# Performance work log

Measured on AMD Instinct MI355X. Metric: run time of the kernel, lower is better.

Reference implementation:

```python
import jax, jax.numpy as jnp
import numpy as np

# ---- static config (matches init_kwargs) ----
B, L, D, H, NC = 2, 4096, 256, 8, 3
TOP_N, R = 8, 32              # top_n, vicinity_radius
LS, LE = 1000, 3000           # label_start, label_end
NL = 2                        # n_cross_attn_layers
FF = 4 * D                    # ffn_expand * d_model
Q_MAX = 2 * TOP_N * (2 * R + 1)  # 1040
HD = D // H


def setup_inputs() -> dict:
    key = jax.random.key(0)
    ks = jax.random.split(key, 12)
    def rn(k, shape, s=0.05):
        return jax.random.normal(k, shape, jnp.float32) * s
    return {
        "encoder_output": jax.random.normal(ks[0], (B, L, D), jnp.float32),
        "coarse_logits": jax.random.normal(ks[1], (B, L, NC), jnp.float32),
        "ln_q_g": jnp.ones((NL, D), jnp.float32),
        "ln_q_b": jnp.zeros((NL, D), jnp.float32),
        "ln_kv_g": jnp.ones((NL, D), jnp.float32),
        "ln_kv_b": jnp.zeros((NL, D), jnp.float32),
        "Wq": rn(ks[2], (NL, D, D)), "bq": jnp.zeros((NL, D), jnp.float32),
        "Wk": rn(ks[3], (NL, D, D)), "bk": jnp.zeros((NL, D), jnp.float32),
        "Wv": rn(ks[4], (NL, D, D)), "bv": jnp.zeros((NL, D), jnp.float32),
        "Wo": rn(ks[5], (NL, D, D)), "bo": jnp.zeros((NL, D), jnp.float32),
        "ffn_g": jnp.ones((NL, D), jnp.float32),
        "ffn_b": jnp.zeros((NL, D), jnp.float32),
        "W1": rn(ks[6], (NL, D, FF)), "b1": jnp.zeros((NL, FF), jnp.float32),
        "W2": rn(ks[7], (NL, FF, D)), "b2": jnp.zeros((NL, D), jnp.float32),
        "head_W": rn(ks[8], (D, NC)), "head_b": jnp.zeros((NC,), jnp.float32),
    }


def _layer_norm(x, g, b, eps=1e-5):
    m = jnp.mean(x, axis=-1, keepdims=True)
    v = jnp.mean(jnp.square(x - m), axis=-1, keepdims=True)
    return (x - m) * jax.lax.rsqrt(v + eps) * g + b


def _select_vicinities(coarse_logits):
    # eval mode: no gumbel noise. Returns (vicinity_idx (B,Q_MAX) int32 with
    # sentinel L at pad/dup slots, q_pad_mask (B,Q_MAX) bool).
    lp = jax.nn.log_softmax(coarse_logits.astype(jnp.float32), axis=-1)
    pos = jnp.arange(L)
    region = (pos >= LS) & (pos < LE)
    acc = jnp.where(region, lp[..., 1], -jnp.inf)
    don = jnp.where(region, lp[..., 2], -jnp.inf)
    _, don_idx = jax.lax.top_k(don, TOP_N)
    _, acc_idx = jax.lax.top_k(acc, TOP_N)
    centers = jnp.concatenate([don_idx, acc_idx], axis=-1)        # (B, 2*TOP_N)
    offsets = jnp.arange(-R, R + 1)
    vic = jnp.clip(centers[:, :, None] + offsets, 0, L - 1).reshape(B, -1)
    s = jnp.sort(vic, axis=-1)
    is_first = jnp.concatenate(
        [jnp.ones((B, 1), bool), s[:, 1:] != s[:, :-1]], axis=-1)
    idx = jnp.where(is_first, s, L)  # sentinel L -> zero row of scratch
    return idx, is_first


def reference(encoder_output, coarse_logits, ln_q_g, ln_q_b, ln_kv_g, ln_kv_b,
              Wq, bq, Wk, bk, Wv, bv, Wo, bo, ffn_g, ffn_b, W1, b1, W2, b2,
              head_W, head_b):
    idx, mask = _select_vicinities(coarse_logits)      # torch.no_grad() region
    idx = jax.lax.stop_gradient(idx)
    mask = jax.lax.stop_gradient(mask)

    scratch = jnp.pad(encoder_output, ((0, 0), (0, 1), (0, 0)))   # (B, L+1, D)
    q_stream = jnp.take_along_axis(scratch, idx[:, :, None], axis=1)  # (B,Q,D)
    kv = encoder_output
    m3 = mask[:, :, None]

    for i in range(NL):
        q_in = _layer_norm(q_stream, ln_q_g[i], ln_q_b[i])
        kv_in = _layer_norm(kv, ln_kv_g[i], ln_kv_b[i])
        q = (q_in @ Wq[i] + bq[i]).reshape(B, Q_MAX, H, HD)
        k = (kv_in @ Wk[i] + bk[i]).reshape(B, L, H, HD)
        v = (kv_in @ Wv[i] + bv[i]).reshape(B, L, H, HD)
        scores = jnp.einsum('bqhd,bkhd->bhqk', q, k) / jnp.sqrt(
            jnp.float32(HD))
        attn = jax.nn.softmax(scores, axis=-1)
        ao = jnp.einsum('bhqk,bkhd->bqhd', attn, v).reshape(B, Q_MAX, D)
        q_stream = q_stream + ao @ Wo[i] + bo[i]
        q_stream = jnp.where(m3, q_stream, 0.0)
        h = _layer_norm(q_stream, ffn_g[i], ffn_b[i])
        h = jax.nn.gelu(h @ W1[i] + b1[i], approximate=False) @ W2[i] + b2[i]
        q_stream = jnp.where(m3, q_stream + h, 0.0)

    out_scratch = scratch.at[jnp.arange(B)[:, None], idx].set(q_stream)
    refined = out_scratch[:, :L]                                  # drop sentinel
    refined_logits = refined @ head_W + head_b                    # (B, L, 3)
    return refined_logits
```

## Files before the change

### kernel.cpp

```cpp
#include <hip/hip_runtime.h>
#include <cmath>

constexpr int B = 2, L = 4096, D = 256, H = 8, NC = 3;
constexpr int TOP_N = 8, R = 32;
constexpr int LS = 1000, LE = 3000;
constexpr int NL = 2;
constexpr int FF = 4 * D;
constexpr int Q_MAX = 2 * TOP_N * (2 * R + 1);
constexpr int HD = D / H;
constexpr int QROWS = B * Q_MAX;
constexpr int KVROWS = B * L;
constexpr int NQT = (Q_MAX + 31) / 32;
constexpr int NREG = LE - LS;
constexpr int NSPLIT = 8;
constexpr int KCHUNK = L / NSPLIT;
constexpr int NT = KCHUNK / 32;

typedef __attribute__((ext_vector_type(8))) short bf16x8;
typedef __attribute__((ext_vector_type(4))) float f32x4;
typedef __attribute__((ext_vector_type(4))) int i32x4;
typedef unsigned short u16;

union fr {
  bf16x8 h;
  i32x4 i;
};

__device__ __forceinline__ u16 f2bs(float f) {
  unsigned int u = __float_as_uint(f);
  unsigned int r = u + 0x7fffu + ((u >> 16) & 1u);
  return (u16)(r >> 16);
}
__device__ __forceinline__ float bs2f(u16 s) {
  return __uint_as_float(((unsigned int)s) << 16);
}
__device__ __forceinline__ float gelu_exact(float x) {
  return 0.5f * x * (1.f + erff(x * 0.70710678118654752440f));
}
__device__ __forceinline__ unsigned cvt_pk(float lo, float hi) {
  unsigned r;
  asm("v_cvt_pk_bf16_f32 %0, %1, %2" : "=v"(r) : "v"(lo), "v"(hi));
  return r;
}

#define GLL16(gsrc, ldst)                                                   \
  __builtin_amdgcn_global_load_lds(                                         \
      (const __attribute__((address_space(1))) unsigned int*)(gsrc),        \
      (__attribute__((address_space(3))) unsigned int*)(ldst), 16, 0, 0)

__global__ __launch_bounds__(1024) void select_kernel(
    const float* __restrict__ logits, int* __restrict__ idx_out,
    int* __restrict__ mask_out) {
  int b = blockIdx.x;
  int tid = threadIdx.x;
  __shared__ float vv[2][NREG];
  __shared__ int centers[2 * TOP_N];
  __shared__ unsigned present[L / 32];
  __shared__ float wred[16];
  __shared__ int wredi[16];
  __shared__ int offs[128];
  __shared__ int wtot[2];

  for (int p = tid; p < NREG; p += 1024) {
    const float* lg = logits + ((long)b * L + LS + p) * NC;
    float x0 = lg[0], x1 = lg[1], x2 = lg[2];
    float m = fmaxf(x0, fmaxf(x1, x2));
    float lse = m + logf(expf(x0 - m) + expf(x1 - m) + expf(x2 - m));
    vv[0][p] = x2 - lse;
    vv[1][p] = x1 - lse;
  }
  if (tid < 128) present[tid] = 0;
  __syncthreads();

  for (int sel = 0; sel < 2; ++sel) {
    for (int t = 0; t < TOP_N; ++t) {
      float bv = -INFINITY;
      int bi = 0x7fffffff;
      for (int p = tid; p < NREG; p += 1024) {
        float x = vv[sel][p];
        if (x > bv || (x == bv && p < bi)) { bv = x; bi = p; }
      }
#pragma unroll
      for (int off = 32; off; off >>= 1) {
        float ov = __shfl_xor(bv, off, 64);
        int oi = __shfl_xor(bi, off, 64);
        if (ov > bv || (ov == bv && oi < bi)) { bv = ov; bi = oi; }
      }
      if ((tid & 63) == 0) { wred[tid >> 6] = bv; wredi[tid >> 6] = bi; }
      __syncthreads();
      if (tid < 64) {
        bv = (tid < 16) ? wred[tid] : -INFINITY;
        bi = (tid < 16) ? wredi[tid] : 0x7fffffff;
#pragma unroll
        for (int off = 8; off; off >>= 1) {
          float ov = __shfl_xor(bv, off, 64);
          int oi = __shfl_xor(bi, off, 64);
          if (ov > bv || (ov == bv && oi < bi)) { bv = ov; bi = oi; }
        }
        if (tid == 0) {
          centers[sel * TOP_N + t] = LS + bi;
          vv[sel][bi] = -INFINITY;
        }
      }
      __syncthreads();
    }
  }

  for (int j = tid; j < Q_MAX; j += 1024) {
    int c = centers[j / (2 * R + 1)];
    int off = j % (2 * R + 1) - R;
    int v = c + off;
    v = v < 0 ? 0 : (v > L - 1 ? L - 1 : v);
    atomicOr(&present[v >> 5], 1u << (v & 31));
  }
  __syncthreads();

  int cnt = (tid < 128) ? __popc(present[tid]) : 0;
  if (tid < 128) {
    int x = cnt;
#pragma unroll
    for (int off = 1; off < 64; off <<= 1) {
      int o = __shfl_up(x, off, 64);
      if ((tid & 63) >= off) x += o;
    }
    if ((tid & 63) == 63) wtot[tid >> 6] = x;
    offs[tid] = x - cnt;
  }
  __syncthreads();
  int total = wtot[0] + wtot[1];
  if (tid < 128) {
    int base = offs[tid] + ((tid >= 64) ? wtot[0] : 0);
    unsigned mword = present[tid];
    while (mword) {
      int i = __ffs(mword) - 1;
      mword &= mword - 1;
      idx_out[b * Q_MAX + base] = tid * 32 + i;
      mask_out[b * Q_MAX + base] = 1;
      ++base;
    }
  }
  for (int j = total + tid; j < Q_MAX; j += 1024) {
    idx_out[b * Q_MAX + j] = L;
    mask_out[b * Q_MAX + j] = 0;
  }
}

__global__ __launch_bounds__(256) void gather_kernel(
    const float* __restrict__ enc, const int* __restrict__ idx,
    float* __restrict__ q_stream) {
  int row = blockIdx.x;
  int b = row / Q_MAX;
  int p = idx[row];
  float v = 0.f;
  if (p < L) v = enc[((long)b * L + p) * D + threadIdx.x];
  q_stream[(long)row * D + threadIdx.x] = v;
}

__global__ __launch_bounds__(256) void ln_bf16(
    const float* __restrict__ in, u16* __restrict__ out,
    const float* __restrict__ gg, const float* __restrict__ bb) {
  long row = blockIdx.x;
  int tid = threadIdx.x;
  float x = in[row * D + tid];
  float s1 = x, s2 = x * x;
#pragma unroll
  for (int off = 32; off; off >>= 1) {
    s1 += __shfl_xor(s1, off, 64);
    s2 += __shfl_xor(s2, off, 64);
  }
  __shared__ float p1[4], p2[4];
  int w = tid >> 6;
  if ((tid & 63) == 0) { p1[w] = s1; p2[w] = s2; }
  __syncthreads();
  s1 = p1[0] + p1[1] + p1[2] + p1[3];
  s2 = p2[0] + p2[1] + p2[2] + p2[3];
  float mean = s1 * (1.f / D);
  float var = fmaxf(s2 * (1.f / D) - mean * mean, 0.f);
  float r = rsqrtf(var + 1e-5f);
  out[row * D + tid] = f2bs((x - mean) * r * gg[tid] + bb[tid]);
}

__global__ __launch_bounds__(256) void ln_kv2(
    const float* __restrict__ in, u16* __restrict__ o0, u16* __restrict__ o1,
    const float* __restrict__ gg, const float* __restrict__ bb) {
  long row = blockIdx.x;
  int tid = threadIdx.x;
  float x = in[row * D + tid];
  float s1 = x, s2 = x * x;
#pragma unroll
  for (int off = 32; off; off >>= 1) {
    s1 += __shfl_xor(s1, off, 64);
    s2 += __shfl_xor(s2, off, 64);
  }
  __shared__ float p1[4], p2[4];
  int w = tid >> 6;
  if ((tid & 63) == 0) { p1[w] = s1; p2[w] = s2; }
  __syncthreads();
  s1 = p1[0] + p1[1] + p1[2] + p1[3];
  s2 = p2[0] + p2[1] + p2[2] + p2[3];
  float mean = s1 * (1.f / D);
  float var = fmaxf(s2 * (1.f / D) - mean * mean, 0.f);
  float r = rsqrtf(var + 1e-5f);
  float xn = (x - mean) * r;
  o0[row * D + tid] = f2bs(xn * gg[tid] + bb[tid]);
  o1[row * D + tid] = f2bs(xn * gg[D + tid] + bb[D + tid]);
}

__global__ __launch_bounds__(256) void transpose_tiled(
    const float* __restrict__ Wq_, const float* __restrict__ Wk_,
    const float* __restrict__ Wv_, const float* __restrict__ Wo_,
    const float* __restrict__ W1_, const float* __restrict__ W2_,
    u16* __restrict__ WT) {
  __shared__ u16 T[64][65];
  const long DD = (long)D * D, DFF = (long)D * FF;
  const long LSTR = 4 * DD + 2 * DFF;
  int t = blockIdx.x;
  int l = t / 192, r = t % 192;
  const float* src;
  long dbase;
  int K_, N_, kt, nt;
  if (r < 64) {
    int which = r >> 4, sub = r & 15;
    kt = sub >> 2;
    nt = sub & 3;
    K_ = 256;
    N_ = 256;
    src = (which == 0 ? Wk_ : which == 1 ? Wv_ : which == 2 ? Wq_ : Wo_) +
          (long)l * DD;
    dbase = (long)l * LSTR + (long)which * DD;
  } else if (r < 128) {
    int sub = r - 64;
    kt = sub >> 4;
    nt = sub & 15;
    K_ = 256;
    N_ = 1024;
    src = W1_ + (long)l * DFF;
    dbase = (long)l * LSTR + 4 * DD;
  } else {
    int sub = r - 128;
    kt = sub >> 2;
    nt = sub & 3;
    K_ = 1024;
    N_ = 256;
    src = W2_ + (long)l * DFF;
    dbase = (long)l * LSTR + 4 * DD + DFF;
  }
  int k0 = kt * 64, n0 = nt * 64;
  {
    int kr = threadIdx.x >> 2, c16 = (threadIdx.x & 3) * 16;
    const float* sp = src + (long)(k0 + kr) * N_ + n0 + c16;
#pragma unroll
    for (int i = 0; i < 4; ++i) {
      float4 v = *reinterpret_cast<const float4*>(sp + 4 * i);
      T[kr][c16 + 4 * i + 0] = f2bs(v.x);
      T[kr][c16 + 4 * i + 1] = f2bs(v.y);
      T[kr][c16 + 4 * i + 2] = f2bs(v.z);
      T[kr][c16 + 4 * i + 3] = f2bs(v.w);
    }
  }
  __syncthreads();
  {
    int nr = threadIdx.x >> 2, kc = (threadIdx.x & 3) * 16;
    u16 tmp[16];
#pragma unroll
    for (int j = 0; j < 16; ++j) tmp[j] = T[kc + j][nr];
    u16* dp = WT + dbase + (long)(n0 + nr) * K_ + k0 + kc;
    *reinterpret_cast<bf16x8*>(dp) = *reinterpret_cast<const bf16x8*>(&tmp[0]);
    *reinterpret_cast<bf16x8*>(dp + 8) =
        *reinterpret_cast<const bf16x8*>(&tmp[8]);
  }
}

template <int EPI>
__global__ __launch_bounds__(256) void gemm_mfma(
    const u16* __restrict__ A, const u16* __restrict__ BT,
    const float* __restrict__ bias, void* __restrict__ Cv,
    const float* __restrict__ resid, const int* __restrict__ mask, int M,
    int N, int K) {
  __shared__ short As[64][40];
  __shared__ short Bs[64][40];
  int bm = blockIdx.y * 64, bn = blockIdx.x * 64;
  int tid = threadIdx.x;
  int lane = tid & 63, w = tid >> 6;
  int g = lane >> 4, li = lane & 15;
  int wr = w >> 1, wc = w & 1;
  f32x4 acc[2][2] = {};

  int srow = tid >> 2, skc = (tid & 3) * 8;
  for (int k0 = 0; k0 < K; k0 += 32) {
    {
      int grow = bm + srow;
      bf16x8 av = {};
      if (grow < M)
        av = *reinterpret_cast<const bf16x8*>(A + (long)grow * K + k0 + skc);
      *reinterpret_cast<bf16x8*>(&As[srow][skc]) = av;
      bf16x8 bv = *reinterpret_cast<const bf16x8*>(
          BT + (long)(bn + srow) * K + k0 + skc);
      *reinterpret_cast<bf16x8*>(&Bs[srow][skc]) = bv;
    }
    __syncthreads();
    bf16x8 a0 = *reinterpret_cast<const bf16x8*>(&As[wr * 32 + li][g * 8]);
    bf16x8 a1 = *reinterpret_cast<const bf16x8*>(&As[wr * 32 + 16 + li][g * 8]);
    bf16x8 b0 = *reinterpret_cast<const bf16x8*>(&Bs[wc * 32 + li][g * 8]);
    bf16x8 b1 = *reinterpret_cast<const bf16x8*>(&Bs[wc * 32 + 16 + li][g * 8]);
    acc[0][0] = __builtin_amdgcn_mfma_f32_16x16x32_bf16(a0, b0, acc[0][0], 0, 0, 0);
    acc[0][1] = __builtin_amdgcn_mfma_f32_16x16x32_bf16(a0, b1, acc[0][1], 0, 0, 0);
    acc[1][0] = __builtin_amdgcn_mfma_f32_16x16x32_bf16(a1, b0, acc[1][0], 0, 0, 0);
    acc[1][1] = __builtin_amdgcn_mfma_f32_16x16x32_bf16(a1, b1, acc[1][1], 0, 0, 0);
    __syncthreads();
  }

#pragma unroll
  for (int mr = 0; mr < 2; ++mr)
#pragma unroll
    for (int nr = 0; nr < 2; ++nr)
#pragma unroll
      for (int r = 0; r < 4; ++r) {
        int row = bm + wr * 32 + mr * 16 + g * 4 + r;
        int col = bn + wc * 32 + nr * 16 + li;
        if (row >= M) continue;
        float v = acc[mr][nr][r] + bias[col];
        if (EPI == 1) v = gelu_exact(v);
        if (EPI == 2) {
          v += resid[(long)row * N + col];
          v = mask[row] ? v : 0.f;
          ((float*)Cv)[(long)row * N + col] = v;
        } else {
          ((u16*)Cv)[(long)row * N + col] = f2bs(v);
        }
      }
}

__global__ __launch_bounds__(256) void gemm_kv(
    const u16* __restrict__ A, const u16* __restrict__ BT,
    const float* __restrict__ biasK, const float* __restrict__ biasV,
    u16* __restrict__ Kh, u16* __restrict__ Vh) {
  __shared__ short As[64][40];
  __shared__ short Bs[64][40];
  int bm = blockIdx.y * 64, bn = blockIdx.x * 64;
  int tid = threadIdx.x;
  int lane = tid & 63, w = tid >> 6;
  int g = lane >> 4, li = lane & 15;
  int wr = w >> 1, wc = w & 1;
  f32x4 acc[2][2] = {};

  int srow = tid >> 2, skc = (tid & 3) * 8;
  for (int k0 = 0; k0 < D; k0 += 32) {
    {
      bf16x8 av = *reinterpret_cast<const bf16x8*>(
          A + (long)(bm + srow) * D + k0 + skc);
      *reinterpret_cast<bf16x8*>(&As[srow][skc]) = av;
      bf16x8 bv = *reinterpret_cast<const bf16x8*>(
          BT + (long)(bn + srow) * D + k0 + skc);
      *reinterpret_cast<bf16x8*>(&Bs[srow][skc]) = bv;
    }
    __syncthreads();
    bf16x8 a0 = *reinterpret_cast<const bf16x8*>(&As[wr * 32 + li][g * 8]);
    bf16x8 a1 = *reinterpret_cast<const bf16x8*>(&As[wr * 32 + 16 + li][g * 8]);
    bf16x8 b0 = *reinterpret_cast<const bf16x8*>(&Bs[wc * 32 + li][g * 8]);
    bf16x8 b1 = *reinterpret_cast<const bf16x8*>(&Bs[wc * 32 + 16 + li][g * 8]);
    acc[0][0] = __builtin_amdgcn_mfma_f32_16x16x32_bf16(a0, b0, acc[0][0], 0, 0, 0);
    acc[0][1] = __builtin_amdgcn_mfma_f32_16x16x32_bf16(a0, b1, acc[0][1], 0, 0, 0);
    acc[1][0] = __builtin_amdgcn_mfma_f32_16x16x32_bf16(a1, b0, acc[1][0], 0, 0, 0);
    acc[1][1] = __builtin_amdgcn_mfma_f32_16x16x32_bf16(a1, b1, acc[1][1], 0, 0, 0);
    __syncthreads();
  }

  if (bn < 256) {
    __shared__ u16 Ct[64][72];
#pragma unroll
    for (int mr = 0; mr < 2; ++mr)
#pragma unroll
      for (int nr = 0; nr < 2; ++nr)
#pragma unroll
        for (int r = 0; r < 4; ++r) {
          int rowL = wr * 32 + mr * 16 + g * 4 + r;
          int colL = wc * 32 + nr * 16 + li;
          Ct[rowL][colL] = f2bs(acc[mr][nr][r] + biasK[bn + colL]);
        }
    __syncthreads();
#pragma unroll
    for (int p = 0; p < 2; ++p) {
      int rowL = (tid >> 3) + p * 32;
      int c8 = (tid & 7) * 8;
      int grow = bm + rowL;
      int b2 = grow >> 12, key = grow & (L - 1);
      int gcol = bn + c8;
      int hh = gcol >> 5, dd = gcol & (HD - 1);
      int cst = (dd >> 3) ^ ((key >> 1) & 3);
      u16* dst = Kh + (((long)(b2 * H + hh) * L + key) * 32 + (cst << 3));
      *reinterpret_cast<bf16x8*>(dst) =
          *reinterpret_cast<const bf16x8*>(&Ct[rowL][c8]);
    }
  } else {
    int vbn = bn - 256;
    __shared__ u16 Ct[64][72];
#pragma unroll
    for (int mr = 0; mr < 2; ++mr)
#pragma unroll
      for (int nr = 0; nr < 2; ++nr)
#pragma unroll
        for (int r = 0; r < 4; ++r) {
          int rowL = wr * 32 + mr * 16 + g * 4 + r;
          int colL = wc * 32 + nr * 16 + li;
          Ct[colL][rowL] = f2bs(acc[mr][nr][r] + biasV[vbn + colL]);
        }
    __syncthreads();
    int b2 = bm >> 12;
#pragma unroll
    for (int p = 0; p < 2; ++p) {
      int colL = (tid >> 3) + p * 32;
      int rem = tid & 7;
      int kb = rem >> 2, k8 = (rem & 3) * 8;
      int gcol = vbn + colL;
      int hh = gcol >> 5, dd = gcol & (HD - 1);
      int kb32 = ((bm & (L - 1)) >> 5) + kb;
      int j = (k8 >> 2) ^ ((dd >> 1) & 6);
      u16* dst = Vh + (((long)(b2 * H + hh) * (L / 32) + kb32) * 1024 +
                       dd * 32 + (j << 2));
      *reinterpret_cast<bf16x8*>(dst) =
          *reinterpret_cast<const bf16x8*>(&Ct[colL][kb * 32 + k8]);
    }
  }
}

constexpr int POOLSZ = NSPLIT * 32 * 33 * 4 + NSPLIT * 32 * 4;

__global__ __launch_bounds__(512) void attn_mfma(
    const u16* __restrict__ Qb, const u16* __restrict__ Kh,
    const u16* __restrict__ Vh, u16* __restrict__ AO) {
  __shared__ alignas(16) char pool[POOLSZ];
  int i = blockIdx.x;
  int xcd = i & 7, slot = i >> 3;
  int bh = (xcd << 1) | (slot >= NQT ? 1 : 0);
  int qt = (slot >= NQT) ? slot - NQT : slot;
  int h = bh & 7;
  int b = bh >> 3;
  int tid = threadIdx.x, w = tid >> 6, lane = tid & 63;
  int g = lane >> 4, li = lane & 15;

  fr qf0, qf1;
  {
    const float QSC = 0.25509836048f;
#pragma unroll
    for (int qb = 0; qb < 2; ++qb) {
      int qrow = qt * 32 + qb * 16 + li;
      if (qrow >= Q_MAX) qrow = Q_MAX - 1;
      bf16x8 raw = *reinterpret_cast<const bf16x8*>(
          Qb + ((long)(b * Q_MAX + qrow)) * D + h * HD + g * 8);
      fr& qf = qb ? qf1 : qf0;
#pragma unroll
      for (int j = 0; j < 4; ++j)
        qf.i[j] = (int)cvt_pk(bs2f((u16)raw[2 * j]) * QSC,
                              bs2f((u16)raw[2 * j + 1]) * QSC);
    }
  }

  f32x4 acc00 = {}, acc01 = {}, acc10 = {}, acc11 = {};
  float den0 = 0.f, den1 = 0.f;
  const f32x4 z = {};

  const u16* kbase = Kh + ((long)(b * H + h) * L) * HD;
  const u16* vbase = Vh + ((long)(b * H + h) * L) * HD;
  int kstart = w * KCHUNK;
  char* wbase = pool + w * 4096;

  int s_li = (li >> 1) & 3;
  int t_li = (li >> 1) & 6;
  int kof0 = li * 32 + ((g ^ s_li) << 3);
  int kof1 = (16 + li) * 32 + ((g ^ s_li) << 3);
  int va0o = li * 32 + ((g ^ t_li) << 2);
  int vb0o = li * 32 + (((4 + g) ^ t_li) << 2);
  int va1o = (16 + li) * 32 + ((g ^ t_li) << 2);
  int vb1o = (16 + li) * 32 + (((4 + g) ^ t_li) << 2);

  for (int t = 0; t < NT; ++t) {
    {
      const u16* ks = kbase + (long)(kstart + t * 32) * HD + lane * 8;
      const u16* vs = vbase + (long)(kstart + t * 32) * HD + lane * 8;
      u16* lk = (u16*)wbase;
      asm volatile("s_waitcnt lgkmcnt(0)" ::: "memory");
      GLL16(ks, lk);
      GLL16(ks + 512, lk + 512);
      GLL16(vs, lk + 1024);
      GLL16(vs + 512, lk + 1536);
      asm volatile("s_waitcnt vmcnt(0)" ::: "memory");
      __builtin_amdgcn_sched_barrier(0);
    }

    const u16* kl = (const u16*)wbase;
    const u16* vl = kl + 1024;
    bf16x8 kf0 = *reinterpret_cast<const bf16x8*>(kl + kof0);
    bf16x8 kf1 = *reinterpret_cast<const bf16x8*>(kl + kof1);
    uint2 va0 = *reinterpret_cast<const uint2*>(vl + va0o);
    uint2 vb0 = *reinterpret_cast<const uint2*>(vl + vb0o);
    uint2 va1 = *reinterpret_cast<const uint2*>(vl + va1o);
    uint2 vb1 = *reinterpret_cast<const uint2*>(vl + vb1o);

    f32x4 s00 = __builtin_amdgcn_mfma_f32_16x16x32_bf16(kf0, qf0.h, z, 0, 0, 0);
    f32x4 s10 = __builtin_amdgcn_mfma_f32_16x16x32_bf16(kf1, qf0.h, z, 0, 0, 0);
    f32x4 s01 = __builtin_amdgcn_mfma_f32_16x16x32_bf16(kf0, qf1.h, z, 0, 0, 0);
    f32x4 s11 = __builtin_amdgcn_mfma_f32_16x16x32_bf16(kf1, qf1.h, z, 0, 0, 0);

    float p00[4], p10[4], p01[4], p11[4];
#pragma unroll
    for (int r = 0; r < 4; ++r) {
      p00[r] = exp2f(s00[r]);
      p10[r] = exp2f(s10[r]);
      p01[r] = exp2f(s01[r]);
      p11[r] = exp2f(s11[r]);
      den0 += p00[r] + p10[r];
      den1 += p01[r] + p11[r];
    }
    fr pf0, pf1;
    pf0.i[0] = (int)cvt_pk(p00[0], p00[1]);
    pf0.i[1] = (int)cvt_pk(p00[2], p00[3]);
    pf0.i[2] = (int)cvt_pk(p10[0], p10[1]);
    pf0.i[3] = (int)cvt_pk(p10[2], p10[3]);
    pf1.i[0] = (int)cvt_pk(p01[0], p01[1]);
    pf1.i[1] = (int)cvt_pk(p01[2], p01[3]);
    pf1.i[2] = (int)cvt_pk(p11[0], p11[1]);
    pf1.i[3] = (int)cvt_pk(p11[2], p11[3]);

    fr v0, v1;
    v0.i = (i32x4){(int)va0.x, (int)va0.y, (int)vb0.x, (int)vb0.y};
    v1.i = (i32x4){(int)va1.x, (int)va1.y, (int)vb1.x, (int)vb1.y};
    acc00 = __builtin_amdgcn_mfma_f32_16x16x32_bf16(v0.h, pf0.h, acc00, 0, 0, 0);
    acc01 = __builtin_amdgcn_mfma_f32_16x16x32_bf16(v0.h, pf1.h, acc01, 0, 0, 0);
    acc10 = __builtin_amdgcn_mfma_f32_16x16x32_bf16(v1.h, pf0.h, acc10, 0, 0, 0);
    acc11 = __builtin_amdgcn_mfma_f32_16x16x32_bf16(v1.h, pf1.h, acc11, 0, 0, 0);
  }

  den0 += __shfl_xor(den0, 16, 64);
  den0 += __shfl_xor(den0, 32, 64);
  den1 += __shfl_xor(den1, 16, 64);
  den1 += __shfl_xor(den1, 32, 64);

  __syncthreads();
  float (*accs)[32][33] = (float(*)[32][33])pool;
  float (*dsh)[32] = (float(*)[32])(pool + NSPLIT * 32 * 33 * 4);
#pragma unroll
  for (int r = 0; r < 4; ++r) {
    accs[w][g * 4 + r][li] = acc00[r];
    accs[w][g * 4 + r][16 + li] = acc01[r];
    accs[w][16 + g * 4 + r][li] = acc10[r];
    accs[w][16 + g * 4 + r][16 + li] = acc11[r];
  }
  if (g == 0) {
    dsh[w][li] = den0;
    dsh[w][16 + li] = den1;
  }
  __syncthreads();

  int q = tid >> 4, dp = tid & 15;
  float Den = 0.f, o0 = 0.f, o1 = 0.f;
#pragma unroll
  for (int ww = 0; ww < NSPLIT; ++ww) {
    Den += dsh[ww][q];
    o0 += accs[ww][2 * dp][q];
    o1 += accs[ww][2 * dp + 1][q];
  }
  float inv = 1.f / Den;
  int qrow = qt * 32 + q;
  if (qrow < Q_MAX) {
    unsigned pk = cvt_pk(o0 * inv, o1 * inv);
    *reinterpret_cast<unsigned*>(
        AO + ((long)(b * Q_MAX + qrow)) * D + h * HD + 2 * dp) = pk;
  }
}

__global__ __launch_bounds__(256) void head_kernel(
    const float* __restrict__ enc, const float* __restrict__ hW,
    const float* __restrict__ hb, float* __restrict__ out) {
  int row = blockIdx.x * 4 + (threadIdx.x >> 6);
  int lane = threadIdx.x & 63;
  const float4 a = *reinterpret_cast<const float4*>(enc + (long)row * D + lane * 4);
  float c0 = 0.f, c1 = 0.f, c2 = 0.f;
  const float av[4] = {a.x, a.y, a.z, a.w};
#pragma unroll
  for (int i = 0; i < 4; ++i) {
    int k = lane * 4 + i;
    c0 += av[i] * hW[k * 3];
    c1 += av[i] * hW[k * 3 + 1];
    c2 += av[i] * hW[k * 3 + 2];
  }
#pragma unroll
  for (int off = 32; off; off >>= 1) {
    c0 += __shfl_down(c0, off, 64);
    c1 += __shfl_down(c1, off, 64);
    c2 += __shfl_down(c2, off, 64);
  }
  if (lane == 0) {
    out[(long)row * 3] = c0 + hb[0];
    out[(long)row * 3 + 1] = c1 + hb[1];
    out[(long)row * 3 + 2] = c2 + hb[2];
  }
}

__global__ __launch_bounds__(64) void overwrite_kernel(
    const float* __restrict__ q_stream, const int* __restrict__ idx,
    const int* __restrict__ mask, const float* __restrict__ hW,
    const float* __restrict__ hb, float* __restrict__ out) {
  int j = blockIdx.x;
  if (!mask[j]) return;
  int b = j / Q_MAX;
  int p = idx[j];
  int lane = threadIdx.x;
  const float* a = q_stream + (long)j * D;
  float a0 = a[lane], a1 = a[lane + 64], a2 = a[lane + 128],
        a3 = a[lane + 192];
  for (int c = 0; c < 3; ++c) {
    float s = a0 * hW[lane * 3 + c] + a1 * hW[(lane + 64) * 3 + c] +
              a2 * hW[(lane + 128) * 3 + c] + a3 * hW[(lane + 192) * 3 + c];
    for (int off = 32; off > 0; off >>= 1) s += __shfl_down(s, off, 64);
    if (lane == 0) out[((long)b * L + p) * 3 + c] = s + hb[c];
  }
}

extern "C" void kernel_launch(void* const* d_in, const int* in_sizes, int n_in,
                              void* d_out, int out_size, void* d_ws,
                              size_t ws_size, hipStream_t stream) {
  const float* enc = (const float*)d_in[0];
  const float* clog = (const float*)d_in[1];
  const float* ln_q_g = (const float*)d_in[2];
  const float* ln_q_b = (const float*)d_in[3];
  const float* ln_kv_g = (const float*)d_in[4];
  const float* ln_kv_b = (const float*)d_in[5];
  const float* Wq = (const float*)d_in[6];
  const float* bq = (const float*)d_in[7];
  const float* Wk = (const float*)d_in[8];
  const float* bk = (const float*)d_in[9];
  const float* Wv = (const float*)d_in[10];
  const float* bv = (const float*)d_in[11];
  const float* Wo = (const float*)d_in[12];
  const float* bo = (const float*)d_in[13];
  const float* ffn_g = (const float*)d_in[14];
  const float* ffn_b = (const float*)d_in[15];
  const float* W1 = (const float*)d_in[16];
  const float* b1 = (const float*)d_in[17];
  const float* W2 = (const float*)d_in[18];
  const float* b2 = (const float*)d_in[19];
  const float* head_W = (const float*)d_in[20];
  const float* head_b = (const float*)d_in[21];
  float* out = (float*)d_out;

  char* ws = (char*)d_ws;
  float* q_stream = (float*)ws;            ws += (long)QROWS * D * 4;
  u16* kvl0 = (u16*)ws;                    ws += (long)KVROWS * D * 2;
  u16* kvl1 = (u16*)ws;                    ws += (long)KVROWS * D * 2;
  u16* Khbuf = (u16*)ws;                   ws += (long)B * H * L * HD * 2;
  u16* Vhbuf = (u16*)ws;                   ws += (long)B * H * L * HD * 2;
  u16* q_ln = (u16*)ws;                    ws += (long)QROWS * D * 2;
  u16* Qbuf = (u16*)ws;                    ws += (long)QROWS * D * 2;
  u16* AObuf = (u16*)ws;                   ws += (long)QROWS * D * 2;
  u16* H1buf = (u16*)ws;                   ws += (long)QROWS * FF * 2;
  u16* WT = (u16*)ws;                      ws += (long)NL * (4 * D * D + 2 * D * FF) * 2;
  int* idxbuf = (int*)ws;                  ws += QROWS * 4;
  int* maskbuf = (int*)ws;

  const long DD = (long)D * D, DFF = (long)D * FF;
  const long LSTR = 4 * DD + 2 * DFF;

  transpose_tiled<<<NL * 192, 256, 0, stream>>>(Wq, Wk, Wv, Wo, W1, W2, WT);
  ln_kv2<<<KVROWS, 256, 0, stream>>>(enc, kvl0, kvl1, ln_kv_g, ln_kv_b);
  select_kernel<<<B, 1024, 0, stream>>>(clog, idxbuf, maskbuf);
  gather_kernel<<<QROWS, 256, 0, stream>>>(enc, idxbuf, q_stream);

  for (int l = 0; l < NL; ++l) {
    u16* base = WT + l * LSTR;
    u16* kv_ln = (l == 0) ? kvl0 : kvl1;

    ln_bf16<<<QROWS, 256, 0, stream>>>(q_stream, q_ln, ln_q_g + l * D, ln_q_b + l * D);

    dim3 gKV(512 / 64, KVROWS / 64);
    gemm_kv<<<gKV, 256, 0, stream>>>(kv_ln, base, bk + l * D, bv + l * D,
                                     Khbuf, Vhbuf);
    dim3 gQ(D / 64, (QROWS + 63) / 64);
    gemm_mfma<0><<<gQ, 256, 0, stream>>>(q_ln, base + 2 * DD, bq + l * D,
                                         (void*)Qbuf, nullptr, nullptr,
                                         QROWS, D, D);

    attn_mfma<<<B * H * NQT, 512, 0, stream>>>(Qbuf, Khbuf, Vhbuf, AObuf);

    gemm_mfma<2><<<gQ, 256, 0, stream>>>(AObuf, base + 3 * DD, bo + l * D,
                                         (void*)q_stream, q_stream, maskbuf,
                                         QROWS, D, D);

    ln_bf16<<<QROWS, 256, 0, stream>>>(q_stream, q_ln, ffn_g + l * D, ffn_b + l * D);
    dim3 gF1(FF / 64, (QROWS + 63) / 64);
    gemm_mfma<1><<<gF1, 256, 0, stream>>>(q_ln, base + 4 * DD, b1 + l * FF,
                                          (void*)H1buf, nullptr, nullptr,
                                          QROWS, FF, D);
    dim3 gF2(D / 64, (QROWS + 63) / 64);
    gemm_mfma<2><<<gF2, 256, 0, stream>>>(H1buf, base + 4 * DD + DFF,
                                          b2 + l * D, (void*)q_stream,
                                          q_stream, maskbuf, QROWS, D, FF);
  }

  head_kernel<<<KVROWS / 4, 256, 0, stream>>>(enc, head_W, head_b, out);
  overwrite_kernel<<<QROWS, 64, 0, stream>>>(q_stream, idxbuf, maskbuf, head_W,
                                             head_b, out);
}
```

Before: 241.0 us.

## Merge Q projection into KV projection launch and speed up top-k selection

The K/V projection GEMM and the Q projection GEMM now run in one launch over a flat block grid, where each block picks its operands and epilogue from its block index. This removes one kernel launch per layer and lets the small Q GEMM run alongside the large K/V GEMM. The top-k selection is also rewritten: each wavefront keeps its values in registers and finds its local top-8 using shuffles, then one wavefront merges the 128 candidates. This replaces 16 block-wide barrier rounds over shared memory.

Measured after the change: 230.5 us. 1.05x faster.

```diff
diff --git a/kernel.cpp b/kernel.cpp
--- a/kernel.cpp
+++ b/kernel.cpp
@@ -15,6 +15,8 @@
 constexpr int NSPLIT = 8;
 constexpr int KCHUNK = L / NSPLIT;
 constexpr int NT = KCHUNK / 32;
+constexpr int KVBLK = 8 * (KVROWS / 64);
+constexpr int QBLK = 4 * ((QROWS + 63) / 64);
 
 typedef __attribute__((ext_vector_type(8))) short bf16x8;
 typedef __attribute__((ext_vector_type(4))) float f32x4;
@@ -53,57 +55,76 @@
     int* __restrict__ mask_out) {
   int b = blockIdx.x;
   int tid = threadIdx.x;
-  __shared__ float vv[2][NREG];
+  int w = tid >> 6, lane = tid & 63;
+  __shared__ float candv[16][8];
+  __shared__ int candi[16][8];
   __shared__ int centers[2 * TOP_N];
   __shared__ unsigned present[L / 32];
-  __shared__ float wred[16];
-  __shared__ int wredi[16];
   __shared__ int offs[128];
   __shared__ int wtot[2];
 
-  for (int p = tid; p < NREG; p += 1024) {
-    const float* lg = logits + ((long)b * L + LS + p) * NC;
-    float x0 = lg[0], x1 = lg[1], x2 = lg[2];
-    float m = fmaxf(x0, fmaxf(x1, x2));
-    float lse = m + logf(expf(x0 - m) + expf(x1 - m) + expf(x2 - m));
-    vv[0][p] = x2 - lse;
-    vv[1][p] = x1 - lse;
+  float vd[2], va[2];
+  int pidx[2];
+#pragma unroll
+  for (int j = 0; j < 2; ++j) {
+    int p = tid + j * 1024;
+    pidx[j] = p;
+    if (p < NREG) {
+      const float* lg = logits + ((long)b * L + LS + p) * NC;
+      float x0 = lg[0], x1 = lg[1], x2 = lg[2];
+      float m = fmaxf(x0, fmaxf(x1, x2));
+      float lse = m + logf(expf(x0 - m) + expf(x1 - m) + expf(x2 - m));
+      vd[j] = x2 - lse;
+      va[j] = x1 - lse;
+    } else {
+      vd[j] = -INFINITY;
+      va[j] = -INFINITY;
+    }
   }
   if (tid < 128) present[tid] = 0;
-  __syncthreads();
 
   for (int sel = 0; sel < 2; ++sel) {
-    for (int t = 0; t < TOP_N; ++t) {
-      float bv = -INFINITY;
-      int bi = 0x7fffffff;
-      for (int p = tid; p < NREG; p += 1024) {
-        float x = vv[sel][p];
-        if (x > bv || (x == bv && p < bi)) { bv = x; bi = p; }
+    float v0 = (sel == 0) ? vd[0] : va[0];
+    float v1 = (sel == 0) ? vd[1] : va[1];
+#pragma unroll
+    for (int r = 0; r < TOP_N; ++r) {
+      float mv;
+      int mi;
+      if (v0 >= v1) { mv = v0; mi = pidx[0]; }
+      else { mv = v1; mi = pidx[1]; }
+#pragma unroll
+      for (int off = 32; off; off >>= 1) {
+        float ov = __shfl_xor(mv, off, 64);
+        int oi = __shfl_xor(mi, off, 64);
+        if (ov > mv || (ov == mv && oi < mi)) { mv = ov; mi = oi; }
       }
-#pragma unroll
-      for (int off = 32; off; off >>= 1) {
-        float ov = __shfl_xor(bv, off, 64);
-        int oi = __shfl_xor(bi, off, 64);
-        if (ov > bv || (ov == bv && oi < bi)) { bv = ov; bi = oi; }
+      if (pidx[0] == mi) v0 = -INFINITY;
+      if (pidx[1] == mi) v1 = -INFINITY;
+      if (lane == 0) { candv[w][r] = mv; candi[w][r] = mi; }
+    }
+    __syncthreads();
+    if (tid < 64) {
+      int j0 = tid, j1 = tid + 64;
+      float c0 = candv[j0 >> 3][j0 & 7], c1 = candv[j1 >> 3][j1 & 7];
+      int i0 = candi[j0 >> 3][j0 & 7], i1 = candi[j1 >> 3][j1 & 7];
+#pragma unroll
+      for (int r = 0; r < TOP_N; ++r) {
+        float mv;
+        int mi;
+        if (c0 > c1 || (c0 == c1 && i0 < i1)) { mv = c0; mi = i0; }
+        else { mv = c1; mi = i1; }
+#pragma unroll
+        for (int off = 32; off; off >>= 1) {
+          float ov = __shfl_xor(mv, off, 64);
+          int oi = __shfl_xor(mi, off, 64);
+          if (ov > mv || (ov == mv && oi < mi)) { mv = ov; mi = oi; }
+        }
+        if (i0 == mi) c0 = -INFINITY;
+        if (i1 == mi) c1 = -INFINITY;
+        if (tid == 0) centers[sel * TOP_N + r] = LS + mi;
       }
-      if ((tid & 63) == 0) { wred[tid >> 6] = bv; wredi[tid >> 6] = bi; }
-      __syncthreads();
-      if (tid < 64) {
-        bv = (tid < 16) ? wred[tid] : -INFINITY;
-        bi = (tid < 16) ? wredi[tid] : 0x7fffffff;
-#pragma unroll
-        for (int off = 8; off; off >>= 1) {
-          float ov = __shfl_xor(bv, off, 64);
-          int oi = __shfl_xor(bi, off, 64);
-          if (ov > bv || (ov == bv && oi < bi)) { bv = ov; bi = oi; }
-        }
-        if (tid == 0) {
-          centers[sel * TOP_N + t] = LS + bi;
-          vv[sel][bi] = -INFINITY;
-        }
-      }
-      __syncthreads();
-    }
+    }
+    __syncthreads();
   }
 
   for (int j = tid; j < Q_MAX; j += 1024) {
@@ -331,24 +352,48 @@
       }
 }
 
-__global__ __launch_bounds__(256) void gemm_kv(
-    const u16* __restrict__ A, const u16* __restrict__ BT,
-    const float* __restrict__ biasK, const float* __restrict__ biasV,
-    u16* __restrict__ Kh, u16* __restrict__ Vh) {
+__global__ __launch_bounds__(256) void gemm_proj(
+    const u16* __restrict__ Akv, const u16* __restrict__ Aq,
+    const u16* __restrict__ WTbase, const float* __restrict__ biasK,
+    const float* __restrict__ biasV, const float* __restrict__ biasQ,
+    u16* __restrict__ Kh, u16* __restrict__ Vh, u16* __restrict__ Qb) {
   __shared__ short As[64][40];
   __shared__ short Bs[64][40];
-  int bm = blockIdx.y * 64, bn = blockIdx.x * 64;
+  __shared__ u16 Ct[64][72];
+  int bid = blockIdx.x;
   int tid = threadIdx.x;
   int lane = tid & 63, w = tid >> 6;
   int g = lane >> 4, li = lane & 15;
   int wr = w >> 1, wc = w & 1;
   f32x4 acc[2][2] = {};
+  const long DD = (long)D * D;
+
+  bool isKV = bid < KVBLK;
+  int bm, bn, M;
+  const u16* A;
+  const u16* BT;
+  if (isKV) {
+    bn = (bid & 7) * 64;
+    bm = (bid >> 3) * 64;
+    M = KVROWS;
+    A = Akv;
+    BT = WTbase;
+  } else {
+    int qb = bid - KVBLK;
+    bn = (qb & 3) * 64;
+    bm = (qb >> 2) * 64;
+    M = QROWS;
+    A = Aq;
+    BT = WTbase + 2 * DD;
+  }
 
   int srow = tid >> 2, skc = (tid & 3) * 8;
   for (int k0 = 0; k0 < D; k0 += 32) {
     {
-      bf16x8 av = *reinterpret_cast<const bf16x8*>(
-          A + (long)(bm + srow) * D + k0 + skc);
+      int grow = bm + srow;
+      bf16x8 av = {};
+      if (grow < M)
+        av = *reinterpret_cast<const bf16x8*>(A + (long)grow * D + k0 + skc);
       *reinterpret_cast<bf16x8*>(&As[srow][skc]) = av;
       bf16x8 bv = *reinterpret_cast<const bf16x8*>(
           BT + (long)(bn + srow) * D + k0 + skc);
@@ -366,8 +411,19 @@
     __syncthreads();
   }
 
-  if (bn < 256) {
-    __shared__ u16 Ct[64][72];
+  if (!isKV) {
+#pragma unroll
+    for (int mr = 0; mr < 2; ++mr)
+#pragma unroll
+      for (int nr = 0; nr < 2; ++nr)
+#pragma unroll
+        for (int r = 0; r < 4; ++r) {
+          int row = bm + wr * 32 + mr * 16 + g * 4 + r;
+          int col = bn + wc * 32 + nr * 16 + li;
+          if (row >= M) continue;
+          Qb[(long)row * D + col] = f2bs(acc[mr][nr][r] + biasQ[col]);
+        }
+  } else if (bn < 256) {
 #pragma unroll
     for (int mr = 0; mr < 2; ++mr)
 #pragma unroll
@@ -394,7 +450,6 @@
     }
   } else {
     int vbn = bn - 256;
-    __shared__ u16 Ct[64][72];
 #pragma unroll
     for (int mr = 0; mr < 2; ++mr)
 #pragma unroll
@@ -672,16 +727,13 @@
 
     ln_bf16<<<QROWS, 256, 0, stream>>>(q_stream, q_ln, ln_q_g + l * D, ln_q_b + l * D);
 
-    dim3 gKV(512 / 64, KVROWS / 64);
-    gemm_kv<<<gKV, 256, 0, stream>>>(kv_ln, base, bk + l * D, bv + l * D,
-                                     Khbuf, Vhbuf);
+    gemm_proj<<<KVBLK + QBLK, 256, 0, stream>>>(
+        kv_ln, q_ln, base, bk + l * D, bv + l * D, bq + l * D, Khbuf, Vhbuf,
+        Qbuf);
+
+    attn_mfma<<<B * H * NQT, 512, 0, stream>>>(Qbuf, Khbuf, Vhbuf, AObuf);
+
     dim3 gQ(D / 64, (QROWS + 63) / 64);
-    gemm_mfma<0><<<gQ, 256, 0, stream>>>(q_ln, base + 2 * DD, bq + l * D,
-                                         (void*)Qbuf, nullptr, nullptr,
-                                         QROWS, D, D);
-
-    attn_mfma<<<B * H * NQT, 512, 0, stream>>>(Qbuf, Khbuf, Vhbuf, AObuf);
-
     gemm_mfma<2><<<gQ, 256, 0, stream>>>(AObuf, base + 3 * DD, bo + l * D,
                                          (void*)q_stream, q_stream, maskbuf,
                                          QROWS, D, D);
```
